# Performance work log

Hardware: AMD Instinct MI355X
Metric: run time of the kernel (lower is better)

## Reference

```python
import jax, jax.numpy as jnp
import numpy as np

GROUPS = 4
SF = 2   # scale_factor
K = 3    # filter_k

def conv1x1(x, w, b):
    return jnp.einsum('bchw,oc->bohw', x, w) + b[None, :, None, None]

def grid_sample(img, grid):
    # img: (N,C,H,W); grid: (N,Hg,Wg,2) xy in [-1,1]; bilinear, border padding, align_corners=False
    N, C, H, W = img.shape
    ix = jnp.clip(((grid[..., 0] + 1.0) * W - 1.0) * 0.5, 0.0, W - 1.0)
    iy = jnp.clip(((grid[..., 1] + 1.0) * H - 1.0) * 0.5, 0.0, H - 1.0)
    x0 = jnp.floor(ix); y0 = jnp.floor(iy)
    wx = (ix - x0)[..., None]; wy = (iy - y0)[..., None]
    x0i = x0.astype(jnp.int32); y0i = y0.astype(jnp.int32)
    x1i = jnp.minimum(x0i + 1, W - 1); y1i = jnp.minimum(y0i + 1, H - 1)
    bidx = jnp.arange(N)[:, None, None]
    v00 = img[bidx, :, y0i, x0i]; v01 = img[bidx, :, y0i, x1i]
    v10 = img[bidx, :, y1i, x0i]; v11 = img[bidx, :, y1i, x1i]   # (N,Hg,Wg,C)
    out = (v00 * (1 - wx) * (1 - wy) + v01 * wx * (1 - wy)
           + v10 * (1 - wx) * wy + v11 * wx * wy)
    return jnp.transpose(out, (0, 3, 1, 2))

def def_sample(x, off):
    b, c, h, w = x.shape
    g = GROUPS
    off = off.reshape(b * g, SF, SF, 2, h, w).transpose(0, 4, 1, 5, 2, 3)
    hd, wd = SF * h, SF * w
    off = off.reshape(b * g, hd, wd, 2)
    gy, gx = jnp.meshgrid(jnp.arange(hd, dtype=x.dtype) + 0.5,
                          jnp.arange(wd, dtype=x.dtype) + 0.5, indexing='ij')
    base = jnp.stack([gx, gy], axis=-1)[None]
    grid = 2.0 * (base + off) / jnp.array([wd, hd], dtype=x.dtype) - 1.0
    return grid_sample(x.reshape(b * g, c // g, h, w), grid).reshape(b, c, hd, wd)

def dyn_filter(x, compress, kw, kb):
    b, c, h, w = x.shape
    kern = jax.nn.softmax(conv1x1(compress, kw, kb), axis=1)  # (b,K*K,h,w)
    p = K // 2
    xp = jnp.pad(x, ((0, 0), (0, 0), (p, p), (p, p)))
    patches = jnp.stack([xp[:, :, dy:dy + h, dx:dx + w]
                         for dy in range(K) for dx in range(K)], axis=2)  # (b,c,K*K,h,w)
    return jnp.einsum('bkhw,bckhw->bchw', kern, patches)

def trim_op(x, toff):
    b, c, h, w = x.shape
    g = GROUPS
    off = toff.reshape(b, g, 2, h, w).transpose(0, 1, 3, 4, 2)  # (b,g,h,w,2) xy
    gy, gx = jnp.meshgrid(jnp.arange(h, dtype=x.dtype) + 0.5,
                          jnp.arange(w, dtype=x.dtype) + 0.5, indexing='ij')
    base = jnp.stack([gx, gy], axis=-1)[None, None]
    grid = (2.0 * (base + off) / jnp.array([w, h], dtype=x.dtype) - 1.0).reshape(b * g, h, w, 2)
    return grid_sample(x.reshape(b * g, c // g, h, w), grid).reshape(b, c, h, w)

def setup_inputs():
    key = jax.random.key(0)
    ks = jax.random.split(key, 13)
    C = 256
    oc = GROUPS * SF * SF * 2  # 32
    f = jnp.float32
    return {
        "x": jax.random.normal(ks[0], (4, C, 64, 64), f),
        "def_off_w": jax.random.normal(ks[1], (oc, C), f) * 0.001,
        "def_off_b": jnp.zeros((oc,), f),
        "def_ast_w": jax.random.normal(ks[2], (oc, C), f) * 0.01,
        "def_ast_b": jnp.zeros((oc,), f),
        "comp_w": jax.random.normal(ks[3], (64, C), f) * (1.0 / np.sqrt(C).astype(np.float32)),
        "comp_b": jnp.zeros((64,), f),
        "filt_w": jax.random.normal(ks[4], (K * K, 64), f) * 0.001,
        "filt_b": jnp.zeros((K * K,), f),
        "trim_w": jax.random.normal(ks[5], (GROUPS * 2, 64), f) * 0.001,
        "trim_b": jnp.zeros((GROUPS * 2,), f),
        "trim_ast_w": jax.random.normal(ks[6], (GROUPS * 2, 64), f) * 0.01,
        "trim_ast_b": jnp.zeros((GROUPS * 2,), f),
    }

def reference(x, def_off_w, def_off_b, def_ast_w, def_ast_b, comp_w, comp_b,
              filt_w, filt_b, trim_w, trim_b, trim_ast_w, trim_ast_b):
    off = conv1x1(x, def_off_w, def_off_b) * jax.nn.sigmoid(conv1x1(x, def_ast_w, def_ast_b))
    x_up = def_sample(x, off)                              # (b,c,2h,2w)
    comp = conv1x1(x_up, comp_w, comp_b)                   # (b,64,2h,2w)
    x_filt = dyn_filter(x_up, comp, filt_w, filt_b)
    toff = conv1x1(comp, trim_w, trim_b) * jax.nn.sigmoid(conv1x1(comp, trim_ast_w, trim_ast_b))
    return trim_op(x_filt, toff)
```

## Files before the change

kernel.cpp:

```cpp
#include <hip/hip_runtime.h>
#include <hip/hip_bf16.h>
#include <string.h>

typedef __hip_bfloat16 bf16;
typedef __attribute__((ext_vector_type(8))) short short8;
typedef __attribute__((ext_vector_type(4))) short short4v;
typedef __attribute__((ext_vector_type(4))) float f32x4;

__device__ __forceinline__ float s2f(short s) {
    return __uint_as_float(((unsigned)(unsigned short)s) << 16);
}
__device__ __forceinline__ short f2s(float v) {
    bf16 t = __float2bfloat16(v); short s; __builtin_memcpy(&s, &t, 2); return s;
}

#define HWD 16384

__global__ __launch_bounds__(512) void k01_xpose_off(const float* __restrict__ x,
        const float* __restrict__ w_off, const float* __restrict__ b_off,
        const float* __restrict__ w_ast, const float* __restrict__ b_ast,
        bf16* __restrict__ xpm, float* __restrict__ offpm)
{
    __shared__ __align__(16) short tileS[64 * 256];
    const int b = blockIdx.x >> 6;
    const int p0 = (blockIdx.x & 63) << 6;
    const int lane = threadIdx.x & 63;
    const int wave = threadIdx.x >> 6;
    const int n = lane & 15, quad = lane >> 4;
    const int wq = wave & 3;
    const int mh = wave >> 2;

    const int j = (wq << 4) + n, oc = j >> 1, kind = j & 1;
    short8 bfrag[8];
    const float* wrow = (kind ? w_ast : w_off) + oc * 256 + quad * 8;
#pragma unroll
    for (int kc = 0; kc < 8; ++kc) {
        float4 lo = *(const float4*)(wrow + kc * 32);
        float4 hi = *(const float4*)(wrow + kc * 32 + 4);
        short8 f;
        f[0] = f2s(lo.x); f[1] = f2s(lo.y); f[2] = f2s(lo.z); f[3] = f2s(lo.w);
        f[4] = f2s(hi.x); f[5] = f2s(hi.y); f[6] = f2s(hi.z); f[7] = f2s(hi.w);
        bfrag[kc] = f;
    }
    float bias = kind ? b_ast[oc] : b_off[oc];

    {
        const float* xb = x + ((size_t)b << 20);
        const int lp = lane;
#pragma unroll
        for (int gg = 0; gg < 4; ++gg) {
            int cbase = (wave << 5) + (gg << 3);
            short8 pk;
#pragma unroll
            for (int jj = 0; jj < 8; ++jj)
                pk[jj] = f2s(xb[((size_t)(cbase + jj) << 12) + p0 + lp]);
            int slot = (cbase >> 3) ^ (lp & 7);
            *(short8*)&tileS[(lp << 8) + (slot << 3)] = pk;
        }
    }
    __syncthreads();

    {
        short* ob = (short*)xpm + ((size_t)((b << 12) + p0) << 8);
#pragma unroll
        for (int rr = 0; rr < 8; ++rr) {
            int r = (wave << 3) + rr;
            short4v v = *(const short4v*)&tileS[(r << 8)
                        + ((((lane >> 1) ^ (r & 7)) << 3) | ((lane & 1) << 2))];
            *(short4v*)(ob + ((size_t)r << 8) + (lane << 2)) = v;
        }
    }

    float* obase = offpm + ((size_t)(b << 12) << 5);
    f32x4 acc0 = {0.f, 0.f, 0.f, 0.f};
    f32x4 acc1 = {0.f, 0.f, 0.f, 0.f};
#pragma unroll
    for (int kc = 0; kc < 8; ++kc) {
        int slot = (((kc << 2) + quad) ^ (n & 7)) << 3;
        short8 a0 = *(const short8*)&tileS[((mh * 32 + n) << 8) + slot];
        short8 a1 = *(const short8*)&tileS[((mh * 32 + 16 + n) << 8) + slot];
        acc0 = __builtin_amdgcn_mfma_f32_16x16x32_bf16(a0, bfrag[kc], acc0, 0, 0, 0);
        acc1 = __builtin_amdgcn_mfma_f32_16x16x32_bf16(a1, bfrag[kc], acc1, 0, 0, 0);
    }
#pragma unroll
    for (int r = 0; r < 4; ++r) {
        float v0 = acc0[r] + bias;
        float v1 = acc1[r] + bias;
        float p0v = __shfl_xor(v0, 1, 64);
        float p1v = __shfl_xor(v1, 1, 64);
        if (!(n & 1)) {
            int px = p0 + mh * 32 + quad * 4 + r;
            obase[((size_t)px << 5) + oc] = v0 * (1.f / (1.f + expf(-p0v)));
            obase[((size_t)(px + 16) << 5) + oc] = v1 * (1.f / (1.f + expf(-p1v)));
        }
    }
}

__global__ __launch_bounds__(512, 4) void k234_defsample_comp_filter(
        const bf16* __restrict__ xpm, const float* __restrict__ offpm,
        const float* __restrict__ cw, const float* __restrict__ cb,
        const float* __restrict__ fw_g, const float* __restrict__ fb,
        const float* __restrict__ tw, const float* __restrict__ tb,
        const float* __restrict__ taw, const float* __restrict__ tab,
        bf16* __restrict__ xfilt, float* __restrict__ toff)
{
    __shared__ __align__(16) short xupS[100 * 256];
    __shared__ __align__(16) float smc[64][65];
    __shared__ __align__(16) float fwS[64 * 12];
    __shared__ __align__(16) float swS[64 * 16];
    __shared__ __align__(16) short kernS[64][24];

    for (int i = threadIdx.x; i < 64 * 12; i += 512) {
        int c = i / 12, k = i % 12;
        fwS[i] = (k < 9) ? fw_g[k * 64 + c] : 0.f;
    }
    for (int i = threadIdx.x; i < 64 * 16; i += 512) {
        int c = i >> 4, jj = i & 15;
        int oc = jj >> 1, kind = jj & 1;
        swS[i] = kind ? taw[oc * 64 + c] : tw[oc * 64 + c];
    }

    const int b = blockIdx.x >> 8;
    const int tile = blockIdx.x & 255;
    const int ty = tile >> 4, tx = tile & 15;
    const int lane = threadIdx.x & 63;
    const int wave = threadIdx.x >> 6;
    const int n = lane & 15, quad = lane >> 4;
    const int wq = wave & 3, mh = wave >> 2;
    const int ocb = wq << 4;

    short8 bfrag[8];
    const float* wrow = cw + (ocb + n) * 256 + quad * 8;
#pragma unroll
    for (int kc = 0; kc < 8; ++kc) {
        float4 lo = *(const float4*)(wrow + kc * 32);
        float4 hi = *(const float4*)(wrow + kc * 32 + 4);
        short8 f;
        f[0] = f2s(lo.x); f[1] = f2s(lo.y); f[2] = f2s(lo.z); f[3] = f2s(lo.w);
        f[4] = f2s(hi.x); f[5] = f2s(hi.y); f[6] = f2s(hi.z); f[7] = f2s(hi.w);
        bfrag[kc] = f;
    }
    float bias = cb[ocb + n];

    {
        const short* xsrc = (const short*)xpm + ((size_t)b << 20);
        const int ph = lane >> 5;
        const int cl = lane & 31;
        const int e = cl << 3;
        const int g = cl >> 3;
        for (int l = (wave << 1) + ph; l < 100; l += 16) {
            int lhy = (l * 205) >> 11;
            int lwx = l - lhy * 10;
            int hy = ty * 8 - 1 + lhy;  hy = min(max(hy, 0), 127);
            int wx = tx * 8 - 1 + lwx;  wx = min(max(wx, 0), 127);
            int h = hy >> 1, w = wx >> 1;
            int och = (g << 3) + ((hy & 1) << 2) + ((wx & 1) << 1);
            const float* orow = offpm + ((size_t)((b << 12) + (h << 6) + w) << 5);
            float ox = orow[och], oy = orow[och + 1];
            float ix = (wx + 0.5f + ox) * 0.5f - 0.5f;
            float iy = (hy + 0.5f + oy) * 0.5f - 0.5f;
            ix = fminf(fmaxf(ix, 0.f), 63.f);
            iy = fminf(fmaxf(iy, 0.f), 63.f);
            float x0f = floorf(ix), y0f = floorf(iy);
            float fx = ix - x0f, fy = iy - y0f;
            int x0 = (int)x0f, y0 = (int)y0f;
            int x1 = min(x0 + 1, 63), y1 = min(y0 + 1, 63);
            float w00 = (1.f - fx) * (1.f - fy), w01 = fx * (1.f - fy);
            float w10 = (1.f - fx) * fy,        w11 = fx * fy;
            short8 v00 = *(const short8*)(xsrc + (((size_t)(y0 << 6) + x0) << 8) + e);
            short8 v01 = *(const short8*)(xsrc + (((size_t)(y0 << 6) + x1) << 8) + e);
            short8 v10 = *(const short8*)(xsrc + (((size_t)(y1 << 6) + x0) << 8) + e);
            short8 v11 = *(const short8*)(xsrc + (((size_t)(y1 << 6) + x1) << 8) + e);
            short8 pk;
#pragma unroll
            for (int jj = 0; jj < 8; ++jj) {
                float v = w00 * s2f(v00[jj]) + w01 * s2f(v01[jj])
                        + w10 * s2f(v10[jj]) + w11 * s2f(v11[jj]);
                pk[jj] = f2s(v);
            }
            int slot = cl ^ (l & 7);
            *(short8*)&xupS[(l << 8) + (slot << 3)] = pk;
        }
    }
    __syncthreads();

    const int m0 = mh << 5;
    const int pA = m0 + n, pB = m0 + 16 + n;
    const int rA = ((pA >> 3) + 1) * 10 + (pA & 7) + 1;
    const int rB = ((pB >> 3) + 1) * 10 + (pB & 7) + 1;
    f32x4 acc0 = {0.f,0.f,0.f,0.f}, acc1 = {0.f,0.f,0.f,0.f};
#pragma unroll
    for (int kc = 0; kc < 8; ++kc) {
        int sp = (kc << 2) + quad;
        short8 a0 = *(const short8*)&xupS[(rA << 8) + ((sp ^ (rA & 7)) << 3)];
        short8 a1 = *(const short8*)&xupS[(rB << 8) + ((sp ^ (rB & 7)) << 3)];
        acc0 = __builtin_amdgcn_mfma_f32_16x16x32_bf16(a0, bfrag[kc], acc0, 0, 0, 0);
        acc1 = __builtin_amdgcn_mfma_f32_16x16x32_bf16(a1, bfrag[kc], acc1, 0, 0, 0);
    }
#pragma unroll
    for (int r = 0; r < 4; ++r) {
        smc[m0 +      quad * 4 + r][ocb + n] = acc0[r] + bias;
        smc[m0 + 16 + quad * 4 + r][ocb + n] = acc1[r] + bias;
    }
    __syncthreads();

    const int px = lane;
    const int q = wave;
    if (q == 0) {
        float a[9];
#pragma unroll
        for (int k = 0; k < 9; ++k) a[k] = fb[k];
        for (int c = 0; c < 64; ++c) {
            float v = smc[px][c];
            const float4* wr = reinterpret_cast<const float4*>(&fwS[c * 12]);
            float4 w0 = wr[0], w1 = wr[1];
            float w8 = fwS[c * 12 + 8];
            a[0] += v * w0.x; a[1] += v * w0.y; a[2] += v * w0.z; a[3] += v * w0.w;
            a[4] += v * w1.x; a[5] += v * w1.y; a[6] += v * w1.z; a[7] += v * w1.w;
            a[8] += v * w8;
        }
        float mx = a[0];
#pragma unroll
        for (int k = 1; k < 9; ++k) mx = fmaxf(mx, a[k]);
        float s = 0.f;
#pragma unroll
        for (int k = 0; k < 9; ++k) { a[k] = expf(a[k] - mx); s += a[k]; }
        float inv = 1.f / s;
#pragma unroll
        for (int k = 0; k < 9; ++k) kernS[px][k] = f2s(a[k] * inv);
    } else if (q <= 4) {
        const int oc0 = (q - 1) << 1;
        float o[2], aa[2];
#pragma unroll
        for (int i = 0; i < 2; ++i) { o[i] = tb[oc0 + i]; aa[i] = tab[oc0 + i]; }
        for (int c = 0; c < 64; ++c) {
            float v = smc[px][c];
            const float* wr = &swS[c << 4];
#pragma unroll
            for (int i = 0; i < 2; ++i) {
                o[i]  += v * wr[2 * (oc0 + i)];
                aa[i] += v * wr[2 * (oc0 + i) + 1];
            }
        }
        int hw = ((ty * 8 + (px >> 3)) << 7) + tx * 8 + (px & 7);
#pragma unroll
        for (int i = 0; i < 2; ++i)
            toff[((size_t)((b << 3) + oc0 + i) << 14) + hw] =
                o[i] * (1.f / (1.f + expf(-aa[i])));
    }
    __syncthreads();

    {
        const int chunk = threadIdx.x & 31;
        const int pxg = threadIdx.x >> 5;
#pragma unroll
        for (int it = 0; it < 4; ++it) {
            int p = (pxg << 2) + it;
            int ly = p >> 3, lx = p & 7;
            int gh = ty * 8 + ly, gw = tx * 8 + lx;
            float wk[9];
            short8 k8 = *(const short8*)&kernS[p][0];
#pragma unroll
            for (int k = 0; k < 8; ++k) wk[k] = s2f(k8[k]);
            wk[8] = s2f(kernS[p][8]);
            float ymask[3] = { gh > 0 ? 1.f : 0.f, 1.f, gh < 127 ? 1.f : 0.f };
            float xmask[3] = { gw > 0 ? 1.f : 0.f, 1.f, gw < 127 ? 1.f : 0.f };
            float sum[8];
#pragma unroll
            for (int jj = 0; jj < 8; ++jj) sum[jj] = 0.f;
#pragma unroll
            for (int dy = 0; dy < 3; ++dy) {
#pragma unroll
                for (int dx = 0; dx < 3; ++dx) {
                    float wgt = wk[dy * 3 + dx] * ymask[dy] * xmask[dx];
                    int r = (ly + dy) * 10 + lx + dx;
                    short8 v = *(const short8*)&xupS[(r << 8)
                                + (((chunk ^ (r & 7))) << 3)];
#pragma unroll
                    for (int jj = 0; jj < 8; ++jj) sum[jj] += wgt * s2f(v[jj]);
                }
            }
            short8 pk;
#pragma unroll
            for (int jj = 0; jj < 8; ++jj) pk[jj] = f2s(sum[jj]);
            int hw = (gh << 7) + gw;
            *(short8*)((short*)xfilt + ((size_t)((b << 14) + hw) << 8)
                       + chunk * 8) = pk;
        }
    }
}

__global__ __launch_bounds__(512, 4) void k6_trim(const bf16* __restrict__ xfilt,
        const float* __restrict__ toff, float* __restrict__ out)
{
    __shared__ __align__(16) float sm[32][260];
    int b = blockIdx.x >> 9;
    int hw0 = (blockIdx.x & 511) << 5;
    int wave = threadIdx.x >> 6, lane = threadIdx.x & 63;
    int ph = lane >> 5;
    int cl = lane & 31;
    int e = cl << 3;
    int g = cl >> 3;
    const short* xb = (const short*)xfilt + ((size_t)(b * HWD) << 8);
    const float* tfx = toff + ((size_t)(b * 8 + 2 * g)     << 14);
    const float* tfy = toff + ((size_t)(b * 8 + 2 * g + 1) << 14);

#pragma unroll
    for (int i = 0; i < 2; ++i) {
        int pp = (wave << 2) + (i << 1) + ph;
        int hw = hw0 + pp;
        int h = hw >> 7, w = hw & 127;
        float ox = tfx[hw], oy = tfy[hw];
        float ix = fminf(fmaxf(w + ox, 0.f), 127.f);
        float iy = fminf(fmaxf(h + oy, 0.f), 127.f);
        float x0f = floorf(ix), y0f = floorf(iy);
        float fx = ix - x0f, fy = iy - y0f;
        int x0 = (int)x0f, y0 = (int)y0f;
        int x1 = min(x0 + 1, 127), y1 = min(y0 + 1, 127);
        float w00 = (1.f - fx) * (1.f - fy), w01 = fx * (1.f - fy);
        float w10 = (1.f - fx) * fy,        w11 = fx * fy;
        short8 v00 = *(const short8*)(xb + (((size_t)(y0 << 7) + x0) << 8) + e);
        short8 v01 = *(const short8*)(xb + (((size_t)(y0 << 7) + x1) << 8) + e);
        short8 v10 = *(const short8*)(xb + (((size_t)(y1 << 7) + x0) << 8) + e);
        short8 v11 = *(const short8*)(xb + (((size_t)(y1 << 7) + x1) << 8) + e);
        float4 lo, hi;
        lo.x = w00 * s2f(v00[0]) + w01 * s2f(v01[0]) + w10 * s2f(v10[0]) + w11 * s2f(v11[0]);
        lo.y = w00 * s2f(v00[1]) + w01 * s2f(v01[1]) + w10 * s2f(v10[1]) + w11 * s2f(v11[1]);
        lo.z = w00 * s2f(v00[2]) + w01 * s2f(v01[2]) + w10 * s2f(v10[2]) + w11 * s2f(v11[2]);
        lo.w = w00 * s2f(v00[3]) + w01 * s2f(v01[3]) + w10 * s2f(v10[3]) + w11 * s2f(v11[3]);
        hi.x = w00 * s2f(v00[4]) + w01 * s2f(v01[4]) + w10 * s2f(v10[4]) + w11 * s2f(v11[4]);
        hi.y = w00 * s2f(v00[5]) + w01 * s2f(v01[5]) + w10 * s2f(v10[5]) + w11 * s2f(v11[5]);
        hi.z = w00 * s2f(v00[6]) + w01 * s2f(v01[6]) + w10 * s2f(v10[6]) + w11 * s2f(v11[6]);
        hi.w = w00 * s2f(v00[7]) + w01 * s2f(v01[7]) + w10 * s2f(v10[7]) + w11 * s2f(v11[7]);
        *(float4*)&sm[pp][e]     = lo;
        *(float4*)&sm[pp][e + 4] = hi;
    }
    __syncthreads();
    int lp = threadIdx.x & 31;
    int cg = threadIdx.x >> 5;
    float* ob = out + ((size_t)b << 22) + hw0 + lp;
#pragma unroll 8
    for (int k = 0; k < 16; ++k) {
        int c = (cg << 4) + k;
        ob[(size_t)c << 14] = sm[lp][c];
    }
}

extern "C" void kernel_launch(void* const* d_in, const int* in_sizes, int n_in,
                              void* d_out, int out_size, void* d_ws, size_t ws_size,
                              hipStream_t stream)
{
    const float* x       = (const float*)d_in[0];
    const float* w_off   = (const float*)d_in[1];
    const float* b_off   = (const float*)d_in[2];
    const float* w_ast   = (const float*)d_in[3];
    const float* b_ast   = (const float*)d_in[4];
    const float* comp_w  = (const float*)d_in[5];
    const float* comp_b  = (const float*)d_in[6];
    const float* filt_w  = (const float*)d_in[7];
    const float* filt_b  = (const float*)d_in[8];
    const float* trim_w  = (const float*)d_in[9];
    const float* trim_b  = (const float*)d_in[10];
    const float* trim_aw = (const float*)d_in[11];
    const float* trim_ab = (const float*)d_in[12];
    float* out = (float*)d_out;

    char* ws = (char*)d_ws;
    float* offpm = (float*)(ws);
    bf16*  xpm   = (bf16*) (ws + (2ull << 20));
    bf16*  xfilt = (bf16*) (ws + (16ull << 20));
    float* toff  = (float*)(ws + (48ull << 20));

    hipLaunchKernelGGL(k01_xpose_off, dim3(256),  dim3(512), 0, stream,
                       x, w_off, b_off, w_ast, b_ast, xpm, offpm);
    hipLaunchKernelGGL(k234_defsample_comp_filter, dim3(1024), dim3(512), 0, stream,
                       xpm, offpm, comp_w, comp_b, filt_w, filt_b,
                       trim_w, trim_b, trim_aw, trim_ab, xfilt, toff);
    hipLaunchKernelGGL(k6_trim,     dim3(2048),  dim3(512), 0, stream,
                       xfilt, toff, out);
}
```

Measured before the change: 170.4 us.

## Split xpose kernel finer, batch offset loads in defsample, widen trim blocks

The first kernel now handles 32 pixels per block instead of 64 and launches twice as many blocks, which gives more parallelism for a small grid of 256 blocks. In the fused defsample kernel, all offset loads are issued up front into a register array before the bilinear gathers, so the dependent global loads are batched and their latency can overlap. The trim kernel moves to 1024 threads per block with one pixel per thread group, a smaller shared-memory pad, and shorter store loops. The cost is more registers and the possibility of bank conflicts from the changed padding.

```diff
diff --git a/kernel.cpp b/kernel.cpp
--- a/kernel.cpp
+++ b/kernel.cpp
@@ -21,9 +21,9 @@
         const float* __restrict__ w_ast, const float* __restrict__ b_ast,
         bf16* __restrict__ xpm, float* __restrict__ offpm)
 {
-    __shared__ __align__(16) short tileS[64 * 256];
-    const int b = blockIdx.x >> 6;
-    const int p0 = (blockIdx.x & 63) << 6;
+    __shared__ __align__(16) short tileS[32 * 256];
+    const int b = blockIdx.x >> 7;
+    const int p0 = (blockIdx.x & 127) << 5;
     const int lane = threadIdx.x & 63;
     const int wave = threadIdx.x >> 6;
     const int n = lane & 15, quad = lane >> 4;
@@ -46,16 +46,18 @@
 
     {
         const float* xb = x + ((size_t)b << 20);
-        const int lp = lane;
-#pragma unroll
-        for (int gg = 0; gg < 4; ++gg) {
-            int cbase = (wave << 5) + (gg << 3);
+        const int px = threadIdx.x & 31;
+        const int gi0 = threadIdx.x >> 5;
+#pragma unroll
+        for (int it = 0; it < 2; ++it) {
+            int gi = gi0 + (it << 4);
+            int cbase = gi << 3;
             short8 pk;
 #pragma unroll
             for (int jj = 0; jj < 8; ++jj)
-                pk[jj] = f2s(xb[((size_t)(cbase + jj) << 12) + p0 + lp]);
-            int slot = (cbase >> 3) ^ (lp & 7);
-            *(short8*)&tileS[(lp << 8) + (slot << 3)] = pk;
+                pk[jj] = f2s(xb[((size_t)(cbase + jj) << 12) + p0 + px]);
+            int slot = gi ^ (px & 7);
+            *(short8*)&tileS[(px << 8) + (slot << 3)] = pk;
         }
     }
     __syncthreads();
@@ -63,8 +65,8 @@
     {
         short* ob = (short*)xpm + ((size_t)((b << 12) + p0) << 8);
 #pragma unroll
-        for (int rr = 0; rr < 8; ++rr) {
-            int r = (wave << 3) + rr;
+        for (int rr = 0; rr < 4; ++rr) {
+            int r = (wave << 2) + rr;
             short4v v = *(const short4v*)&tileS[(r << 8)
                         + ((((lane >> 1) ^ (r & 7)) << 3) | ((lane & 1) << 2))];
             *(short4v*)(ob + ((size_t)r << 8) + (lane << 2)) = v;
@@ -72,26 +74,20 @@
     }
 
     float* obase = offpm + ((size_t)(b << 12) << 5);
-    f32x4 acc0 = {0.f, 0.f, 0.f, 0.f};
-    f32x4 acc1 = {0.f, 0.f, 0.f, 0.f};
+    f32x4 acc = {0.f, 0.f, 0.f, 0.f};
 #pragma unroll
     for (int kc = 0; kc < 8; ++kc) {
         int slot = (((kc << 2) + quad) ^ (n & 7)) << 3;
-        short8 a0 = *(const short8*)&tileS[((mh * 32 + n) << 8) + slot];
-        short8 a1 = *(const short8*)&tileS[((mh * 32 + 16 + n) << 8) + slot];
-        acc0 = __builtin_amdgcn_mfma_f32_16x16x32_bf16(a0, bfrag[kc], acc0, 0, 0, 0);
-        acc1 = __builtin_amdgcn_mfma_f32_16x16x32_bf16(a1, bfrag[kc], acc1, 0, 0, 0);
+        short8 a = *(const short8*)&tileS[((mh * 16 + n) << 8) + slot];
+        acc = __builtin_amdgcn_mfma_f32_16x16x32_bf16(a, bfrag[kc], acc, 0, 0, 0);
     }
 #pragma unroll
     for (int r = 0; r < 4; ++r) {
-        float v0 = acc0[r] + bias;
-        float v1 = acc1[r] + bias;
+        float v0 = acc[r] + bias;
         float p0v = __shfl_xor(v0, 1, 64);
-        float p1v = __shfl_xor(v1, 1, 64);
         if (!(n & 1)) {
-            int px = p0 + mh * 32 + quad * 4 + r;
+            int px = p0 + mh * 16 + quad * 4 + r;
             obase[((size_t)px << 5) + oc] = v0 * (1.f / (1.f + expf(-p0v)));
-            obase[((size_t)(px + 16) << 5) + oc] = v1 * (1.f / (1.f + expf(-p1v)));
         }
     }
 }
@@ -148,38 +144,55 @@
         const int cl = lane & 31;
         const int e = cl << 3;
         const int g = cl >> 3;
-        for (int l = (wave << 1) + ph; l < 100; l += 16) {
-            int lhy = (l * 205) >> 11;
-            int lwx = l - lhy * 10;
-            int hy = ty * 8 - 1 + lhy;  hy = min(max(hy, 0), 127);
-            int wx = tx * 8 - 1 + lwx;  wx = min(max(wx, 0), 127);
-            int h = hy >> 1, w = wx >> 1;
-            int och = (g << 3) + ((hy & 1) << 2) + ((wx & 1) << 1);
-            const float* orow = offpm + ((size_t)((b << 12) + (h << 6) + w) << 5);
-            float ox = orow[och], oy = orow[och + 1];
-            float ix = (wx + 0.5f + ox) * 0.5f - 0.5f;
-            float iy = (hy + 0.5f + oy) * 0.5f - 0.5f;
-            ix = fminf(fmaxf(ix, 0.f), 63.f);
-            iy = fminf(fmaxf(iy, 0.f), 63.f);
-            float x0f = floorf(ix), y0f = floorf(iy);
-            float fx = ix - x0f, fy = iy - y0f;
-            int x0 = (int)x0f, y0 = (int)y0f;
-            int x1 = min(x0 + 1, 63), y1 = min(y0 + 1, 63);
-            float w00 = (1.f - fx) * (1.f - fy), w01 = fx * (1.f - fy);
-            float w10 = (1.f - fx) * fy,        w11 = fx * fy;
-            short8 v00 = *(const short8*)(xsrc + (((size_t)(y0 << 6) + x0) << 8) + e);
-            short8 v01 = *(const short8*)(xsrc + (((size_t)(y0 << 6) + x1) << 8) + e);
-            short8 v10 = *(const short8*)(xsrc + (((size_t)(y1 << 6) + x0) << 8) + e);
-            short8 v11 = *(const short8*)(xsrc + (((size_t)(y1 << 6) + x1) << 8) + e);
-            short8 pk;
-#pragma unroll
-            for (int jj = 0; jj < 8; ++jj) {
-                float v = w00 * s2f(v00[jj]) + w01 * s2f(v01[jj])
-                        + w10 * s2f(v10[jj]) + w11 * s2f(v11[jj]);
-                pk[jj] = f2s(v);
+        const int base = (wave << 1) + ph;
+
+        float2 fo[7];
+#pragma unroll
+        for (int it = 0; it < 7; ++it) {
+            int l = base + (it << 4);
+            if (l < 100) {
+                int lhy = (l * 205) >> 11;
+                int lwx = l - lhy * 10;
+                int hy = min(max(ty * 8 - 1 + lhy, 0), 127);
+                int wx = min(max(tx * 8 - 1 + lwx, 0), 127);
+                int och = (g << 3) + ((hy & 1) << 2) + ((wx & 1) << 1);
+                fo[it] = *(const float2*)(offpm
+                        + ((size_t)((b << 12) + ((hy >> 1) << 6) + (wx >> 1)) << 5)
+                        + och);
             }
-            int slot = cl ^ (l & 7);
-            *(short8*)&xupS[(l << 8) + (slot << 3)] = pk;
+        }
+#pragma unroll
+        for (int it = 0; it < 7; ++it) {
+            int l = base + (it << 4);
+            if (l < 100) {
+                int lhy = (l * 205) >> 11;
+                int lwx = l - lhy * 10;
+                int hy = min(max(ty * 8 - 1 + lhy, 0), 127);
+                int wx = min(max(tx * 8 - 1 + lwx, 0), 127);
+                float ix = (wx + 0.5f + fo[it].x) * 0.5f - 0.5f;
+                float iy = (hy + 0.5f + fo[it].y) * 0.5f - 0.5f;
+                ix = fminf(fmaxf(ix, 0.f), 63.f);
+                iy = fminf(fmaxf(iy, 0.f), 63.f);
+                float x0f = floorf(ix), y0f = floorf(iy);
+                float fx = ix - x0f, fy = iy - y0f;
+                int x0 = (int)x0f, y0 = (int)y0f;
+                int x1 = min(x0 + 1, 63), y1 = min(y0 + 1, 63);
+                float w00 = (1.f - fx) * (1.f - fy), w01 = fx * (1.f - fy);
+                float w10 = (1.f - fx) * fy,        w11 = fx * fy;
+                short8 v00 = *(const short8*)(xsrc + (((size_t)(y0 << 6) + x0) << 8) + e);
+                short8 v01 = *(const short8*)(xsrc + (((size_t)(y0 << 6) + x1) << 8) + e);
+                short8 v10 = *(const short8*)(xsrc + (((size_t)(y1 << 6) + x0) << 8) + e);
+                short8 v11 = *(const short8*)(xsrc + (((size_t)(y1 << 6) + x1) << 8) + e);
+                short8 pk;
+#pragma unroll
+                for (int jj = 0; jj < 8; ++jj) {
+                    float v = w00 * s2f(v00[jj]) + w01 * s2f(v01[jj])
+                            + w10 * s2f(v10[jj]) + w11 * s2f(v11[jj]);
+                    pk[jj] = f2s(v);
+                }
+                int slot = cl ^ (l & 7);
+                *(short8*)&xupS[(l << 8) + (slot << 3)] = pk;
+            }
         }
     }
     __syncthreads();
@@ -290,24 +303,21 @@
     }
 }
 
-__global__ __launch_bounds__(512, 4) void k6_trim(const bf16* __restrict__ xfilt,
+__global__ __launch_bounds__(1024, 4) void k6_trim(const bf16* __restrict__ xfilt,
         const float* __restrict__ toff, float* __restrict__ out)
 {
-    __shared__ __align__(16) float sm[32][260];
+    __shared__ __align__(16) float sm[32][258];
     int b = blockIdx.x >> 9;
     int hw0 = (blockIdx.x & 511) << 5;
-    int wave = threadIdx.x >> 6, lane = threadIdx.x & 63;
-    int ph = lane >> 5;
-    int cl = lane & 31;
+    int pp = threadIdx.x >> 5;
+    int cl = threadIdx.x & 31;
     int e = cl << 3;
     int g = cl >> 3;
     const short* xb = (const short*)xfilt + ((size_t)(b * HWD) << 8);
     const float* tfx = toff + ((size_t)(b * 8 + 2 * g)     << 14);
     const float* tfy = toff + ((size_t)(b * 8 + 2 * g + 1) << 14);
 
-#pragma unroll
-    for (int i = 0; i < 2; ++i) {
-        int pp = (wave << 2) + (i << 1) + ph;
+    {
         int hw = hw0 + pp;
         int h = hw >> 7, w = hw & 127;
         float ox = tfx[hw], oy = tfy[hw];
@@ -323,25 +333,23 @@
         short8 v01 = *(const short8*)(xb + (((size_t)(y0 << 7) + x1) << 8) + e);
         short8 v10 = *(const short8*)(xb + (((size_t)(y1 << 7) + x0) << 8) + e);
         short8 v11 = *(const short8*)(xb + (((size_t)(y1 << 7) + x1) << 8) + e);
-        float4 lo, hi;
-        lo.x = w00 * s2f(v00[0]) + w01 * s2f(v01[0]) + w10 * s2f(v10[0]) + w11 * s2f(v11[0]);
-        lo.y = w00 * s2f(v00[1]) + w01 * s2f(v01[1]) + w10 * s2f(v10[1]) + w11 * s2f(v11[1]);
-        lo.z = w00 * s2f(v00[2]) + w01 * s2f(v01[2]) + w10 * s2f(v10[2]) + w11 * s2f(v11[2]);
-        lo.w = w00 * s2f(v00[3]) + w01 * s2f(v01[3]) + w10 * s2f(v10[3]) + w11 * s2f(v11[3]);
-        hi.x = w00 * s2f(v00[4]) + w01 * s2f(v01[4]) + w10 * s2f(v10[4]) + w11 * s2f(v11[4]);
-        hi.y = w00 * s2f(v00[5]) + w01 * s2f(v01[5]) + w10 * s2f(v10[5]) + w11 * s2f(v11[5]);
-        hi.z = w00 * s2f(v00[6]) + w01 * s2f(v01[6]) + w10 * s2f(v10[6]) + w11 * s2f(v11[6]);
-        hi.w = w00 * s2f(v00[7]) + w01 * s2f(v01[7]) + w10 * s2f(v10[7]) + w11 * s2f(v11[7]);
-        *(float4*)&sm[pp][e]     = lo;
-        *(float4*)&sm[pp][e + 4] = hi;
+#pragma unroll
+        for (int jp = 0; jp < 4; ++jp) {
+            float2 t;
+            t.x = w00 * s2f(v00[2*jp])   + w01 * s2f(v01[2*jp])
+                + w10 * s2f(v10[2*jp])   + w11 * s2f(v11[2*jp]);
+            t.y = w00 * s2f(v00[2*jp+1]) + w01 * s2f(v01[2*jp+1])
+                + w10 * s2f(v10[2*jp+1]) + w11 * s2f(v11[2*jp+1]);
+            *(float2*)&sm[pp][e + 2*jp] = t;
+        }
     }
     __syncthreads();
     int lp = threadIdx.x & 31;
     int cg = threadIdx.x >> 5;
     float* ob = out + ((size_t)b << 22) + hw0 + lp;
-#pragma unroll 8
-    for (int k = 0; k < 16; ++k) {
-        int c = (cg << 4) + k;
+#pragma unroll
+    for (int k = 0; k < 8; ++k) {
+        int c = (cg << 3) + k;
         ob[(size_t)c << 14] = sm[lp][c];
     }
 }
@@ -371,11 +379,11 @@
     bf16*  xfilt = (bf16*) (ws + (16ull << 20));
     float* toff  = (float*)(ws + (48ull << 20));
 
-    hipLaunchKernelGGL(k01_xpose_off, dim3(256),  dim3(512), 0, stream,
+    hipLaunchKernelGGL(k01_xpose_off, dim3(512),  dim3(512), 0, stream,
                        x, w_off, b_off, w_ast, b_ast, xpm, offpm);
     hipLaunchKernelGGL(k234_defsample_comp_filter, dim3(1024), dim3(512), 0, stream,
                        xpm, offpm, comp_w, comp_b, filt_w, filt_b,
                        trim_w, trim_b, trim_aw, trim_ab, xfilt, toff);
-    hipLaunchKernelGGL(k6_trim,     dim3(2048),  dim3(512), 0, stream,
+    hipLaunchKernelGGL(k6_trim,     dim3(2048),  dim3(1024), 0, stream,
                        xfilt, toff, out);
 }
```

Measured after the change: 174.4 us. 1.02x slower.
